# Performance work log

Measured on AMD Instinct MI355X. Metric: run time of the kernel, lower is better.

The kernel has to match this reference:

```python
import jax, jax.numpy as jnp
import numpy as np

LOG2 = 16          # log2_num_embeddings
VQ_DIM = 32        # vq_dim
EMB_DIM = 512      # embedding_dim
TEMPERATURE = 1.0
EPS = 1e-8


def setup_inputs() -> dict:
    key = jax.random.key(0)
    k = jax.random.split(key, 7)
    h = jax.random.normal(k[0], (32, 2048, EMB_DIM), dtype=jnp.float32)
    attn_mask = jax.random.randint(k[1], (32, 2048), 0, 2).astype(jnp.int32)
    # proj: Linear(EMB_DIM, VQ_DIM); stored as [in, out]
    W_proj = jax.random.normal(k[2], (EMB_DIM, VQ_DIM), dtype=jnp.float32) * 0.02
    b_proj = jnp.zeros((VQ_DIM,), dtype=jnp.float32)
    # proj_inv: Linear(VQ_DIM, EMB_DIM); stored as [in, out]
    W_inv = jax.random.normal(k[3], (VQ_DIM, EMB_DIM), dtype=jnp.float32) * 0.02
    b_inv = jnp.zeros((EMB_DIM,), dtype=jnp.float32)
    # codebook: 2*LOG2 rows of VQ_DIM
    emb = jax.random.normal(k[4], (2 * LOG2, VQ_DIM), dtype=jnp.float32)
    return {"h": h, "attn_mask": attn_mask, "W_proj": W_proj, "b_proj": b_proj,
            "W_inv": W_inv, "b_inv": b_inv, "emb": emb}


def reference(h, attn_mask, W_proj, b_proj, W_inv, b_inv, emb):
    B, L, _ = h.shape
    M = 2 * LOG2
    # project + L2-normalize (with eps, as in forward)
    hp = jnp.einsum('ble,ed->bld', h, W_proj) + b_proj
    hn = hp / (jnp.linalg.norm(hp, axis=-1, keepdims=True) + EPS)
    # normalize codebook rows (with eps, as in forward)
    E = emb / (jnp.linalg.norm(emb, axis=-1, keepdims=True) + EPS)
    # pairwise squared distances [B, L, M]
    d = (jnp.sum(hn * hn, axis=-1, keepdims=True)
         + jnp.sum(E * E, axis=-1)
         - 2.0 * jnp.einsum('bld,md->blm', hn, E))
    # group-wise (pairs of 2) softmax
    dp = d.reshape(B, L, LOG2, 2)
    A = jax.nn.softmax(-dp / TEMPERATURE, axis=-1)            # [B, L, LOG2, 2]
    code = jnp.argmax(A, axis=-1)                              # [B, L, LOG2] int
    # train mode: soft assignment h_vq = A @ E
    h_vq = jnp.einsum('blm,md->bld', A.reshape(B, L, M), E)    # [B, L, VQ_DIM]
    mask = (attn_mask == 1)
    quantized = jnp.where(mask[..., None], h_vq, 0.0)
    quantized = jnp.einsum('bld,de->ble', quantized, W_inv) + b_inv
    # binary code -> integer id, zeroed at masked-out positions
    shift = 2 ** jnp.arange(LOG2, dtype=jnp.int64)
    vq_code = jnp.where(mask, jnp.sum(code.astype(jnp.int64) * shift, axis=-1), 0)
    vq_loss = jnp.float32(0.0)
    return quantized, vq_code, vq_loss
```

## Files before the change

kernel.cpp:

```cpp
#include <hip/hip_runtime.h>
#include <math.h>

#define EMB 512
#define VQ 32
#define MCODES 32
#define EPS 1e-8f

__global__ __launch_bounds__(256)
void prep_kernel(const float* __restrict__ emb, const float* __restrict__ W_inv,
                 float* __restrict__ Cw, float* __restrict__ G, float* __restrict__ qv,
                 float* __restrict__ loss_out) {
  const int b = blockIdx.x;
  const int tid = threadIdx.x;
  __shared__ float En_s[VQ];
  float ss = 0.f;
#pragma unroll
  for (int d = 0; d < VQ; ++d) { float v = emb[b * VQ + d]; ss += v * v; }
  const float inv = 1.0f / (sqrtf(ss) + EPS);
  if (tid < VQ) En_s[tid] = emb[b * VQ + tid] * inv;
  __syncthreads();
  float a0 = 0.f, a1 = 0.f;
#pragma unroll 8
  for (int d = 0; d < VQ; ++d) {
    const float en = En_s[d];
    const float2 wv = ((const float2*)(W_inv + d * EMB))[tid];
    a0 += en * wv.x;
    a1 += en * wv.y;
  }
  ((float2*)(Cw + b * EMB))[tid] = make_float2(a0, a1);
  if (tid < VQ) G[b * VQ + tid] = 2.0f * En_s[tid];
  if (tid == 0) {
    float qq = 0.f;
#pragma unroll
    for (int d = 0; d < VQ; ++d) qq += En_s[d] * En_s[d];
    qv[b] = qq;
    if (b == 0) loss_out[0] = 0.0f;
  }
}

__global__ __launch_bounds__(256)
void proj_kernel(const float* __restrict__ h, const int* __restrict__ mask,
                 const float* __restrict__ W_proj, const float* __restrict__ b_proj,
                 const float* __restrict__ G, const float* __restrict__ qv,
                 float* __restrict__ Aout, float* __restrict__ code_out) {
  const int tid = threadIdx.x;
  const int wv = tid >> 6;
  const int lane = tid & 63;
  const int slot = lane >> 3;
  const int dg = lane & 7;
  const int tile = blockIdx.x * 32;
  __shared__ float hp_s[4][32][36];

  const float4* __restrict__ h4 = (const float4*)h;
  const float4* __restrict__ W4 = (const float4*)W_proj;

  const int e4base = wv * 32;
  const float4* hr0 = h4 + (size_t)(tile + slot) * (EMB / 4) + e4base;
  const float4* hr1 = hr0 + 8 * (EMB / 4);
  const float4* hr2 = hr1 + 8 * (EMB / 4);
  const float4* hr3 = hr2 + 8 * (EMB / 4);

  float4 a0 = make_float4(0.f, 0.f, 0.f, 0.f), a1 = a0, a2 = a0, a3 = a0;

  for (int e4 = 0; e4 < 32; ++e4) {
    const int eb = (e4base + e4) << 2;
    const float4 w0 = W4[(eb + 0) * 8 + dg];
    const float4 w1 = W4[(eb + 1) * 8 + dg];
    const float4 w2 = W4[(eb + 2) * 8 + dg];
    const float4 w3 = W4[(eb + 3) * 8 + dg];
    const float4 v0 = hr0[e4];
    const float4 v1 = hr1[e4];
    const float4 v2 = hr2[e4];
    const float4 v3 = hr3[e4];
#define ACC4(A, V)                                                        \
    A.x += V.x * w0.x; A.x += V.y * w1.x; A.x += V.z * w2.x; A.x += V.w * w3.x; \
    A.y += V.x * w0.y; A.y += V.y * w1.y; A.y += V.z * w2.y; A.y += V.w * w3.y; \
    A.z += V.x * w0.z; A.z += V.y * w1.z; A.z += V.z * w2.z; A.z += V.w * w3.z; \
    A.w += V.x * w0.w; A.w += V.y * w1.w; A.w += V.z * w2.w; A.w += V.w * w3.w;
    ACC4(a0, v0) ACC4(a1, v1) ACC4(a2, v2) ACC4(a3, v3)
#undef ACC4
  }
  *(float4*)&hp_s[wv][slot     ][dg * 4] = a0;
  *(float4*)&hp_s[wv][slot +  8][dg * 4] = a1;
  *(float4*)&hp_s[wv][slot + 16][dg * 4] = a2;
  *(float4*)&hp_s[wv][slot + 24][dg * 4] = a3;
  __syncthreads();

  if (tid < 32) {
    const int t = tile + tid;
    const float4* bp4 = (const float4*)b_proj;
    float4 hp[8];
    float ssum = 0.f;
#pragma unroll
    for (int k = 0; k < 8; ++k) {
      float4 p0 = *(const float4*)&hp_s[0][tid][k * 4];
      const float4 p1 = *(const float4*)&hp_s[1][tid][k * 4];
      const float4 p2 = *(const float4*)&hp_s[2][tid][k * 4];
      const float4 p3 = *(const float4*)&hp_s[3][tid][k * 4];
      const float4 b = bp4[k];
      float4 v;
      v.x = ((p0.x + p1.x) + p2.x) + p3.x + b.x;
      v.y = ((p0.y + p1.y) + p2.y) + p3.y + b.y;
      v.z = ((p0.z + p1.z) + p2.z) + p3.z + b.z;
      v.w = ((p0.w + p1.w) + p2.w) + p3.w + b.w;
      hp[k] = v;
      ssum += v.x * v.x + v.y * v.y + v.z * v.z + v.w * v.w;
    }
    const float inv = 1.0f / (sqrtf(ssum) + EPS);
#pragma unroll
    for (int k = 0; k < 8; ++k) {
      hp[k].x *= inv; hp[k].y *= inv; hp[k].z *= inv; hp[k].w *= inv;
    }
    const float4* G4 = (const float4*)G;
    float av[32];
    int code = 0;
#pragma unroll
    for (int g = 0; g < 16; ++g) {
      float d0 = 0.f, d1 = 0.f;
#pragma unroll
      for (int k = 0; k < 8; ++k) {
        const float4 g0 = G4[(2 * g) * 8 + k];
        const float4 g1 = G4[(2 * g + 1) * 8 + k];
        const float4 hv = hp[k];
        d0 += hv.x * g0.x + hv.y * g0.y + hv.z * g0.z + hv.w * g0.w;
        d1 += hv.x * g1.x + hv.y * g1.y + hv.z * g1.z + hv.w * g1.w;
      }
      const float s0 = d0 - qv[2 * g];
      const float s1 = d1 - qv[2 * g + 1];
      const float mx = fmaxf(s0, s1);
      const float e0 = expf(s0 - mx);
      const float e1 = expf(s1 - mx);
      const float rs = 1.0f / (e0 + e1);
      av[2 * g] = e0 * rs;
      av[2 * g + 1] = e1 * rs;
      code |= (e1 > e0) ? (1 << g) : 0;
    }
    const int mk = mask[t];
    const float msk = (mk == 1) ? 1.0f : 0.0f;
    float4* Ao = (float4*)(Aout + (size_t)t * MCODES);
#pragma unroll
    for (int k = 0; k < 8; ++k) {
      Ao[k] = make_float4(av[4 * k] * msk, av[4 * k + 1] * msk,
                          av[4 * k + 2] * msk, av[4 * k + 3] * msk);
    }
    code_out[t] = (mk == 1) ? (float)code : 0.0f;
  }
}

__global__ __launch_bounds__(256)
void inv_kernel(const float* __restrict__ Ap, const float* __restrict__ Cw,
                const float* __restrict__ b_inv, float* __restrict__ qout) {
  const int tid = threadIdx.x;
  const int w = tid >> 6;
  const int lane = tid & 63;
  const int ep = w * 64 + lane;
  const int tile = blockIdx.x * 64;
  float2 c[32];
#pragma unroll
  for (int m = 0; m < 32; ++m) c[m] = ((const float2*)(Cw + m * EMB))[ep];
  const float2 bi = ((const float2*)b_inv)[ep];
  for (int tt = 0; tt < 64; ++tt) {
    const int t = tile + tt;
    const float4* a4 = (const float4*)(Ap + (size_t)t * 32);
    float accx = bi.x, accy = bi.y;
#pragma unroll
    for (int k = 0; k < 8; ++k) {
      const float4 a = a4[k];
      accx += a.x * c[4 * k].x + a.y * c[4 * k + 1].x + a.z * c[4 * k + 2].x + a.w * c[4 * k + 3].x;
      accy += a.x * c[4 * k].y + a.y * c[4 * k + 1].y + a.z * c[4 * k + 2].y + a.w * c[4 * k + 3].y;
    }
    ((float2*)(qout + (size_t)t * EMB))[ep] = make_float2(accx, accy);
  }
}

extern "C" void kernel_launch(void* const* d_in, const int* in_sizes, int n_in,
                              void* d_out, int out_size, void* d_ws, size_t ws_size,
                              hipStream_t stream) {
  (void)n_in; (void)out_size; (void)ws_size;
  const float* h      = (const float*)d_in[0];
  const int*   mask   = (const int*)  d_in[1];
  const float* W_proj = (const float*)d_in[2];
  const float* b_proj = (const float*)d_in[3];
  const float* W_inv  = (const float*)d_in[4];
  const float* b_inv  = (const float*)d_in[5];
  const float* emb    = (const float*)d_in[6];

  const int N = in_sizes[1];

  float* quant    = (float*)d_out;
  float* code_out = quant + (size_t)N * EMB;
  float* loss_out = code_out + N;

  float* ws = (float*)d_ws;
  float* Ap = ws;
  float* Cw = Ap + (size_t)N * MCODES;
  float* G  = Cw + MCODES * EMB;
  float* qv = G + MCODES * VQ;

  prep_kernel<<<MCODES, 256, 0, stream>>>(emb, W_inv, Cw, G, qv, loss_out);
  proj_kernel<<<N / 32, 256, 0, stream>>>(h, mask, W_proj, b_proj, G, qv, Ap, code_out);
  inv_kernel<<<N / 64, 256, 0, stream>>>(Ap, Cw, b_inv, quant);
}
```

Before: 130.6 us.

## Stage h tile through padded LDS with coalesced loads and halve rows per block

The projection kernel now loads a 16-token tile of h into padded shared memory with fully coalesced float4 loads, then computes partial dot products from LDS instead of strided per-lane global reads. The block handles 16 tokens instead of 32, doubling the grid and reusing the LDS buffer for the cross-wave reduction. This targets poor coalescing of the 128 MB h read, at the cost of halving W_proj reuse per block and adding syncs and LDS traffic.

```diff
diff --git a/kernel.cpp b/kernel.cpp
--- a/kernel.cpp
+++ b/kernel.cpp
@@ -5,6 +5,12 @@
 #define VQ 32
 #define MCODES 32
 #define EPS 1e-8f
+
+#define ACC4(A, V)                                                        \
+    A.x += V.x * w0.x; A.x += V.y * w1.x; A.x += V.z * w2.x; A.x += V.w * w3.x; \
+    A.y += V.x * w0.y; A.y += V.y * w1.y; A.y += V.z * w2.y; A.y += V.w * w3.y; \
+    A.z += V.x * w0.z; A.z += V.y * w1.z; A.z += V.z * w2.z; A.z += V.w * w3.z; \
+    A.w += V.x * w0.w; A.w += V.y * w1.w; A.w += V.z * w2.w; A.w += V.w * w3.w;
 
 __global__ __launch_bounds__(256)
 void prep_kernel(const float* __restrict__ emb, const float* __restrict__ W_inv,
@@ -48,55 +54,53 @@
   const int lane = tid & 63;
   const int slot = lane >> 3;
   const int dg = lane & 7;
-  const int tile = blockIdx.x * 32;
-  __shared__ float hp_s[4][32][36];
+  const int tile = blockIdx.x * 16;
+
+  __shared__ float4 hlds[16 * 129];
 
   const float4* __restrict__ h4 = (const float4*)h;
+  const float4* hsrc = h4 + (size_t)tile * (EMB / 4);
+#pragma unroll
+  for (int k = 0; k < 8; ++k) {
+    const int g = k * 256 + tid;
+    hlds[(g >> 7) * 129 + (g & 127)] = hsrc[g];
+  }
+  __syncthreads();
+
   const float4* __restrict__ W4 = (const float4*)W_proj;
-
   const int e4base = wv * 32;
-  const float4* hr0 = h4 + (size_t)(tile + slot) * (EMB / 4) + e4base;
-  const float4* hr1 = hr0 + 8 * (EMB / 4);
-  const float4* hr2 = hr1 + 8 * (EMB / 4);
-  const float4* hr3 = hr2 + 8 * (EMB / 4);
-
-  float4 a0 = make_float4(0.f, 0.f, 0.f, 0.f), a1 = a0, a2 = a0, a3 = a0;
+
+  float4 acc0 = make_float4(0.f, 0.f, 0.f, 0.f), acc1 = acc0;
 
   for (int e4 = 0; e4 < 32; ++e4) {
+    const float4 v0 = hlds[slot * 129 + e4base + e4];
+    const float4 v1 = hlds[(slot + 8) * 129 + e4base + e4];
     const int eb = (e4base + e4) << 2;
     const float4 w0 = W4[(eb + 0) * 8 + dg];
     const float4 w1 = W4[(eb + 1) * 8 + dg];
     const float4 w2 = W4[(eb + 2) * 8 + dg];
     const float4 w3 = W4[(eb + 3) * 8 + dg];
-    const float4 v0 = hr0[e4];
-    const float4 v1 = hr1[e4];
-    const float4 v2 = hr2[e4];
-    const float4 v3 = hr3[e4];
-#define ACC4(A, V)                                                        \
-    A.x += V.x * w0.x; A.x += V.y * w1.x; A.x += V.z * w2.x; A.x += V.w * w3.x; \
-    A.y += V.x * w0.y; A.y += V.y * w1.y; A.y += V.z * w2.y; A.y += V.w * w3.y; \
-    A.z += V.x * w0.z; A.z += V.y * w1.z; A.z += V.z * w2.z; A.z += V.w * w3.z; \
-    A.w += V.x * w0.w; A.w += V.y * w1.w; A.w += V.z * w2.w; A.w += V.w * w3.w;
-    ACC4(a0, v0) ACC4(a1, v1) ACC4(a2, v2) ACC4(a3, v3)
-#undef ACC4
-  }
-  *(float4*)&hp_s[wv][slot     ][dg * 4] = a0;
-  *(float4*)&hp_s[wv][slot +  8][dg * 4] = a1;
-  *(float4*)&hp_s[wv][slot + 16][dg * 4] = a2;
-  *(float4*)&hp_s[wv][slot + 24][dg * 4] = a3;
-  __syncthreads();
-
-  if (tid < 32) {
+    ACC4(acc0, v0) ACC4(acc1, v1)
+  }
+
+  __syncthreads();
+
+  float* part = (float*)hlds;
+  *(float4*)&part[(wv * 16 + slot) * 36 + dg * 4] = acc0;
+  *(float4*)&part[(wv * 16 + slot + 8) * 36 + dg * 4] = acc1;
+  __syncthreads();
+
+  if (tid < 16) {
     const int t = tile + tid;
     const float4* bp4 = (const float4*)b_proj;
     float4 hp[8];
     float ssum = 0.f;
 #pragma unroll
     for (int k = 0; k < 8; ++k) {
-      float4 p0 = *(const float4*)&hp_s[0][tid][k * 4];
-      const float4 p1 = *(const float4*)&hp_s[1][tid][k * 4];
-      const float4 p2 = *(const float4*)&hp_s[2][tid][k * 4];
-      const float4 p3 = *(const float4*)&hp_s[3][tid][k * 4];
+      const float4 p0 = *(const float4*)&part[(0 * 16 + tid) * 36 + k * 4];
+      const float4 p1 = *(const float4*)&part[(1 * 16 + tid) * 36 + k * 4];
+      const float4 p2 = *(const float4*)&part[(2 * 16 + tid) * 36 + k * 4];
+      const float4 p3 = *(const float4*)&part[(3 * 16 + tid) * 36 + k * 4];
       const float4 b = bp4[k];
       float4 v;
       v.x = ((p0.x + p1.x) + p2.x) + p3.x + b.x;
@@ -198,6 +202,6 @@
   float* qv = G + MCODES * VQ;
 
   prep_kernel<<<MCODES, 256, 0, stream>>>(emb, W_inv, Cw, G, qv, loss_out);
-  proj_kernel<<<N / 32, 256, 0, stream>>>(h, mask, W_proj, b_proj, G, qv, Ap, code_out);
+  proj_kernel<<<N / 16, 256, 0, stream>>>(h, mask, W_proj, b_proj, G, qv, Ap, code_out);
   inv_kernel<<<N / 64, 256, 0, stream>>>(Ap, Cw, b_inv, quant);
 }
```

New measurement: 150.0 us. 14.9% more time.
